# Optimization experiments

Hardware: AMD Instinct MI355X
Metric: run time of the kernel (lower is better)

Reference implementation:

```python
import jax, jax.numpy as jnp
import numpy as np

E = 200_000   # number of edges (messages)
T = 500_000   # number of triplets
H = 128       # hidden_channels
B = 8         # num_bilinear
R = 6         # num_radial
S = 7         # num_spherical


def setup_inputs() -> dict:
    key = jax.random.key(0)
    ks = jax.random.split(key, 18)
    w = 0.05  # small init scale for numerical stability
    return {
        "x":   jax.random.normal(ks[0], (E, H), dtype=jnp.float32),
        "rbf": jax.random.normal(ks[1], (E, R), dtype=jnp.float32),
        "sbf": jax.random.normal(ks[2], (T, S * R), dtype=jnp.float32),
        "idx_kj": jax.random.randint(ks[3], (T,), 0, E),
        "idx_ji": jax.random.randint(ks[4], (T,), 0, E),
        # parameters (stored as [in, out] so we apply x @ w)
        "lin_rbf_w": jax.random.normal(ks[5], (R, H), dtype=jnp.float32) * w,
        "lin_sbf_w": jax.random.normal(ks[6], (S * R, B), dtype=jnp.float32) * w,
        "lin_kj_w": jax.random.normal(ks[7], (H, H), dtype=jnp.float32) * w,
        "lin_kj_b": jnp.zeros((H,), dtype=jnp.float32),
        "lin_ji_w": jax.random.normal(ks[8], (H, H), dtype=jnp.float32) * w,
        "lin_ji_b": jnp.zeros((H,), dtype=jnp.float32),
        "W": jax.random.normal(ks[9], (H, B, H), dtype=jnp.float32) * (2.0 / H),
        "before_w": jax.random.normal(ks[10], (1, 2, H, H), dtype=jnp.float32) * w,
        "before_b": jnp.zeros((1, 2, H), dtype=jnp.float32),
        "lin_w": jax.random.normal(ks[11], (H, H), dtype=jnp.float32) * w,
        "lin_b": jnp.zeros((H,), dtype=jnp.float32),
        "after_w": jax.random.normal(ks[12], (2, 2, H, H), dtype=jnp.float32) * w,
        "after_b": jnp.zeros((2, 2, H), dtype=jnp.float32),
    }


def _residual(h, w2, b2):
    # DimeNet ResidualLayer: h + act(lin2(act(lin1(h))))
    return h + jax.nn.silu(jax.nn.silu(h @ w2[0] + b2[0]) @ w2[1] + b2[1])


def reference(x, rbf, sbf, idx_kj, idx_ji,
              lin_rbf_w, lin_sbf_w, lin_kj_w, lin_kj_b,
              lin_ji_w, lin_ji_b, W,
              before_w, before_b, lin_w, lin_b, after_w, after_b):
    act = jax.nn.silu
    rbf_p = rbf @ lin_rbf_w                     # [E, H]
    sbf_p = sbf @ lin_sbf_w                     # [T, B]
    x_ji = act(x @ lin_ji_w + lin_ji_b)         # [E, H]
    x_kj = act(x @ lin_kj_w + lin_kj_b) * rbf_p # [E, H]
    g = x_kj[idx_kj]                            # gather -> [T, H]
    # bilinear: 'wj,wl,ijl->wi' with i,l=hidden, j=bilinear
    m = jnp.einsum('wj,wl,ijl->wi', sbf_p, g, W)  # [T, H]
    agg = jax.ops.segment_sum(m, idx_ji, num_segments=x.shape[0])  # [E, H]
    h = x_ji + agg
    for i in range(before_w.shape[0]):
        h = _residual(h, before_w[i], before_b[i])
    h = act(h @ lin_w + lin_b) + x
    for i in range(after_w.shape[0]):
        h = _residual(h, after_w[i], after_b[i])
    return h
```

## Files before the change

kernel.cpp:

```cpp
#include <hip/hip_runtime.h>

#define E_N 200000
#define T_N 500000

typedef __attribute__((ext_vector_type(8))) short bf16x8;
typedef __attribute__((ext_vector_type(4))) float f32x4;
typedef unsigned short u16;
typedef unsigned int u32;

#define SWZ(b) ((b) ^ ((((b) >> 8) & 7) << 4))

__device__ __forceinline__ u16 f2bf(float f){
  u32 u = __float_as_uint(f);
  return (u16)((u + 0x7fffu + ((u >> 16) & 1u)) >> 16);
}
__device__ __forceinline__ float silu_f(float v){
  return __fdividef(v, 1.f + __expf(-v));
}
__device__ __forceinline__ void gl_lds16(const void* g, void* l){
  __builtin_amdgcn_global_load_lds((const __attribute__((address_space(1))) u32*)g,
                                   (__attribute__((address_space(3))) u32*)l, 16, 0, 0);
}

__device__ __forceinline__ void gemm_tile(const char* ldsA, const char* ldsB,
                                          int wv, int lane, f32x4 acc[8]){
  const int arow = wv*16 + (lane & 15);
  const int kof = (lane >> 4) << 3;
  #pragma unroll
  for (int kc = 0; kc < 4; kc++){
    const int kb = (kc*32 + kof)*2;
    bf16x8 a = *(const bf16x8*)(ldsA + SWZ(arow*256 + kb));
    #pragma unroll
    for (int n = 0; n < 8; n++){
      bf16x8 b = *(const bf16x8*)(ldsB + SWZ((n*16 + (lane & 15))*256 + kb));
      acc[n] = __builtin_amdgcn_mfma_f32_16x16x32_bf16(a, b, acc[n], 0, 0, 0);
    }
  }
}

__global__ __launch_bounds__(256) void k_cvt_W(const float* __restrict__ W, u16* __restrict__ out){
  int i = blockIdx.x*256 + threadIdx.x;
  out[i] = f2bf(W[i]);
}

__global__ __launch_bounds__(256) void k_cvt_T(const float* __restrict__ jiw, const float* __restrict__ kjw,
                                               const float* __restrict__ bw, const float* __restrict__ lw,
                                               const float* __restrict__ aw, u16* __restrict__ out){
  int i = blockIdx.x*256 + threadIdx.x;
  int m = i >> 14, o = i & 16383;
  int n = o >> 7, k = o & 127;
  const float* src;
  switch (m){
    case 0: src = jiw; break;
    case 1: src = kjw; break;
    case 2: src = bw; break;
    case 3: src = bw + 16384; break;
    case 4: src = lw; break;
    default: src = aw + (m - 5)*16384; break;
  }
  out[i] = f2bf(src[k*128 + n]);
}

__global__ __launch_bounds__(256) void k_edge(const float* __restrict__ x, const float* __restrict__ rbf,
    const float* __restrict__ rbfw, const u16* __restrict__ wji, const u16* __restrict__ wkj,
    const float* __restrict__ bji, const float* __restrict__ bkj,
    float* __restrict__ out, u16* __restrict__ xkj)
{
  __shared__ __align__(16) char ldsA[16384];
  __shared__ __align__(16) char ldsB[32768];
  __shared__ float lrbf[64*6];
  __shared__ float lrbfw[6*128];
  __shared__ float lbj[128];
  __shared__ float lbk[128];
  const int tid = threadIdx.x;
  const int e0 = blockIdx.x * 64;

  #pragma unroll
  for (int it = 0; it < 4; it++){
    int i = it*256 + tid;
    int row = i >> 4, c8 = (i & 15) << 3;
    const float4* s = (const float4*)(x + (e0 + row)*128 + c8);
    float4 v0 = s[0], v1 = s[1];
    union { u16 us[8]; uint4 q; } u;
    u.us[0]=f2bf(v0.x); u.us[1]=f2bf(v0.y); u.us[2]=f2bf(v0.z); u.us[3]=f2bf(v0.w);
    u.us[4]=f2bf(v1.x); u.us[5]=f2bf(v1.y); u.us[6]=f2bf(v1.z); u.us[7]=f2bf(v1.w);
    *(uint4*)(ldsA + SWZ(row*256 + c8*2)) = u.q;
  }
  #pragma unroll
  for (int it = 0; it < 8; it++){
    int p = (it*256 + tid)*16;
    int pb = __builtin_amdgcn_readfirstlane(p);
    int n = p >> 8, o = p & 255;
    gl_lds16((const char*)wji + n*256 + (o ^ ((n & 7) << 4)), ldsB + pb);
  }
  for (int i = tid; i < 384; i += 256) lrbf[i] = rbf[e0*6 + i];
  for (int i = tid; i < 768; i += 256) lrbfw[i] = rbfw[i];
  if (tid < 128){ lbj[tid] = bji[tid]; lbk[tid] = bkj[tid]; }
  __syncthreads();

  const int wv = tid >> 6, lane = tid & 63;
  const int colb = lane & 15, rgrp = (lane >> 4) << 2;
  f32x4 acc[8];
  #pragma unroll
  for (int n = 0; n < 8; n++)
    #pragma unroll
    for (int r = 0; r < 4; r++) acc[n][r] = 0.f;
  gemm_tile(ldsA, ldsB, wv, lane, acc);
  #pragma unroll
  for (int n = 0; n < 8; n++){
    int col = n*16 + colb;
    float b = lbj[col];
    #pragma unroll
    for (int r = 0; r < 4; r++){
      int row = e0 + wv*16 + rgrp + r;
      out[row*128 + col] = silu_f(acc[n][r] + b);
    }
  }
  __syncthreads();
  #pragma unroll
  for (int it = 0; it < 8; it++){
    int p = (it*256 + tid)*16;
    int pb = __builtin_amdgcn_readfirstlane(p);
    int n = p >> 8, o = p & 255;
    gl_lds16((const char*)wkj + n*256 + (o ^ ((n & 7) << 4)), ldsB + pb);
  }
  __syncthreads();
  #pragma unroll
  for (int n = 0; n < 8; n++)
    #pragma unroll
    for (int r = 0; r < 4; r++) acc[n][r] = 0.f;
  gemm_tile(ldsA, ldsB, wv, lane, acc);

  float rb[4][6];
  #pragma unroll
  for (int r = 0; r < 4; r++)
    #pragma unroll
    for (int c = 0; c < 6; c++) rb[r][c] = lrbf[(wv*16 + rgrp + r)*6 + c];
  #pragma unroll
  for (int n = 0; n < 8; n++){
    int col = n*16 + colb;
    float b = lbk[col];
    float wc[6];
    #pragma unroll
    for (int c = 0; c < 6; c++) wc[c] = lrbfw[c*128 + col];
    #pragma unroll
    for (int r = 0; r < 4; r++){
      float rp = 0.f;
      #pragma unroll
      for (int c = 0; c < 6; c++) rp += rb[r][c]*wc[c];
      int row = e0 + wv*16 + rgrp + r;
      xkj[row*128 + col] = f2bf(silu_f(acc[n][r] + b) * rp);
    }
  }
}

__global__ __launch_bounds__(512) void k_trip(
    const u16* __restrict__ xkj, const float* __restrict__ sbf, const float* __restrict__ sbfw,
    const int* __restrict__ idx_kj, const int* __restrict__ idx_ji, const u16* __restrict__ Wbf,
    float* __restrict__ out)
{
  __shared__ __align__(16) char ldsG[32768];
  __shared__ __align__(16) char ldsB[32768];
  __shared__ float lss[128*8];
  __shared__ int lji[128];
  __shared__ int lkj[128];
  const int tid = threadIdx.x;
  const int t0 = blockIdx.x * 128;

  {
    float* lsbf = (float*)ldsB;
    for (int i = tid; i < 128*42; i += 512){
      int gi = t0*42 + i;
      lsbf[i] = (gi < T_N*42) ? sbf[gi] : 0.f;
    }
  }
  if (tid < 128){
    int w = t0 + tid;
    lji[tid] = (w < T_N) ? idx_ji[w] : -1;
    lkj[tid] = (w < T_N) ? idx_kj[w] : 0;
  }
  __syncthreads();
  #pragma unroll
  for (int it = 0; it < 4; it++){
    int p = (it*512 + tid)*16;
    int pb = __builtin_amdgcn_readfirstlane(p);
    int w = p >> 8, o = p & 255;
    gl_lds16((const char*)xkj + lkj[w]*256 + (o ^ ((w & 7) << 4)), ldsG + pb);
  }
  {
    const float* lsbf = (const float*)ldsB;
    if (tid < 128){
      float a[8];
      #pragma unroll
      for (int k = 0; k < 8; k++) a[k] = 0.f;
      for (int c = 0; c < 42; c++){
        float v = lsbf[tid*42 + c];
        #pragma unroll
        for (int k = 0; k < 8; k++) a[k] += v * sbfw[c*8 + k];
      }
      #pragma unroll
      for (int k = 0; k < 8; k++) lss[tid*8 + k] = a[k];
    }
  }
  __syncthreads();
  #pragma unroll
  for (int it = 0; it < 4; it++){
    int p = (it*512 + tid)*16;
    int pb = __builtin_amdgcn_readfirstlane(p);
    int n = p >> 8, o = p & 255;
    gl_lds16((const char*)Wbf + n*2048 + (o ^ ((n & 7) << 4)), ldsB + pb);
  }
  __syncthreads();

  const int wv = tid >> 6, lane = tid & 63;
  const int rowl = wv*16 + (lane & 15);
  const int kof = (lane >> 4) << 3;
  f32x4 acc[8];
  #pragma unroll
  for (int n = 0; n < 8; n++)
    #pragma unroll
    for (int r = 0; r < 4; r++) acc[n][r] = 0.f;

  for (int j = 0; j < 8; j++){
    const float s = lss[rowl*8 + j];
    #pragma unroll
    for (int kc = 0; kc < 4; kc++){
      const int kb = (kc*32 + kof)*2;
      union { bf16x8 v; u32 u[4]; } ga, aa;
      ga.v = *(const bf16x8*)(ldsG + SWZ(rowl*256 + kb));
      #pragma unroll
      for (int q = 0; q < 4; q++){
        float lo = __uint_as_float(ga.u[q] << 16) * s;
        float hi = __uint_as_float(ga.u[q] & 0xffff0000u) * s;
        asm("v_cvt_pk_bf16_f32 %0, %1, %2" : "=v"(aa.u[q]) : "v"(lo), "v"(hi));
      }
      #pragma unroll
      for (int n = 0; n < 8; n++){
        bf16x8 b = *(const bf16x8*)(ldsB + SWZ((n*16 + (lane & 15))*256 + kb));
        acc[n] = __builtin_amdgcn_mfma_f32_16x16x32_bf16(aa.v, b, acc[n], 0, 0, 0);
      }
    }
    if (j < 7){
      __syncthreads();
      #pragma unroll
      for (int it = 0; it < 4; it++){
        int p = (it*512 + tid)*16;
        int pb = __builtin_amdgcn_readfirstlane(p);
        int n = p >> 8, o = p & 255;
        gl_lds16((const char*)Wbf + n*2048 + (j + 1)*256 + (o ^ ((n & 7) << 4)), ldsB + pb);
      }
      __syncthreads();
    }
  }
  const int colb = lane & 15, rgrp = (lane >> 4) << 2;
  #pragma unroll
  for (int n = 0; n < 8; n++){
    const int col = n*16 + colb;
    #pragma unroll
    for (int r = 0; r < 4; r++){
      int e = lji[wv*16 + rgrp + r];
      if (e >= 0) unsafeAtomicAdd(out + e*128 + col, acc[n][r]);
    }
  }
}

__global__ __launch_bounds__(256) void k_epi(
    const float* __restrict__ x, float* __restrict__ hio, const u16* __restrict__ wm,
    const float* __restrict__ bb2, const float* __restrict__ linb, const float* __restrict__ ab2)
{
  __shared__ __align__(16) char ldsA[16384];
  __shared__ __align__(16) char ldsB[32768];
  __shared__ float lbias[7][128];
  const int tid = threadIdx.x;
  const int e0 = blockIdx.x * 64;
  if (tid < 128){
    lbias[0][tid] = bb2[tid];
    lbias[1][tid] = bb2[128 + tid];
    lbias[2][tid] = linb[tid];
    lbias[3][tid] = ab2[tid];
    lbias[4][tid] = ab2[128 + tid];
    lbias[5][tid] = ab2[256 + tid];
    lbias[6][tid] = ab2[384 + tid];
  }
  const int wv = tid >> 6, lane = tid & 63;
  const int colb = lane & 15, rgrp = (lane >> 4) << 2;
  float h[8][4], t[8][4];
  f32x4 acc[8];
  #pragma unroll
  for (int n = 0; n < 8; n++)
    #pragma unroll
    for (int r = 0; r < 4; r++)
      h[n][r] = hio[(e0 + wv*16 + rgrp + r)*128 + n*16 + colb];

#define STAGE_B(mi) { \
  _Pragma("unroll") \
  for (int it = 0; it < 8; it++){ \
    int p = (it*256 + tid)*16; \
    int pb = __builtin_amdgcn_readfirstlane(p); \
    int nn = p >> 8, o = p & 255; \
    gl_lds16((const char*)wm + (mi)*32768 + nn*256 + (o ^ ((nn & 7) << 4)), ldsB + pb); \
  } }
#define WRITE_A(v) { \
  _Pragma("unroll") \
  for (int n = 0; n < 8; n++){ \
    _Pragma("unroll") \
    for (int r = 0; r < 4; r++){ \
      int rowl = wv*16 + rgrp + r; \
      *(u16*)(ldsA + SWZ(rowl*256 + (n*16 + colb)*2)) = f2bf(v[n][r]); \
    } } }
#define RUN_GEMM() { \
  _Pragma("unroll") \
  for (int n = 0; n < 8; n++){ \
    _Pragma("unroll") \
    for (int r = 0; r < 4; r++) acc[n][r] = 0.f; } \
  gemm_tile(ldsA, ldsB, wv, lane, acc); }

  STAGE_B(0); WRITE_A(h); __syncthreads(); RUN_GEMM();
  #pragma unroll
  for (int n = 0; n < 8; n++){ float b = lbias[0][n*16 + colb];
    #pragma unroll
    for (int r = 0; r < 4; r++) t[n][r] = silu_f(acc[n][r] + b); }
  __syncthreads(); STAGE_B(1); WRITE_A(t); __syncthreads(); RUN_GEMM();
  #pragma unroll
  for (int n = 0; n < 8; n++){ float b = lbias[1][n*16 + colb];
    #pragma unroll
    for (int r = 0; r < 4; r++) h[n][r] += silu_f(acc[n][r] + b); }
  __syncthreads(); STAGE_B(2); WRITE_A(h); __syncthreads(); RUN_GEMM();
  #pragma unroll
  for (int n = 0; n < 8; n++){ float b = lbias[2][n*16 + colb];
    #pragma unroll
    for (int r = 0; r < 4; r++)
      h[n][r] = silu_f(acc[n][r] + b) + x[(e0 + wv*16 + rgrp + r)*128 + n*16 + colb]; }
  __syncthreads(); STAGE_B(3); WRITE_A(h); __syncthreads(); RUN_GEMM();
  #pragma unroll
  for (int n = 0; n < 8; n++){ float b = lbias[3][n*16 + colb];
    #pragma unroll
    for (int r = 0; r < 4; r++) t[n][r] = silu_f(acc[n][r] + b); }
  __syncthreads(); STAGE_B(4); WRITE_A(t); __syncthreads(); RUN_GEMM();
  #pragma unroll
  for (int n = 0; n < 8; n++){ float b = lbias[4][n*16 + colb];
    #pragma unroll
    for (int r = 0; r < 4; r++) h[n][r] += silu_f(acc[n][r] + b); }
  __syncthreads(); STAGE_B(5); WRITE_A(h); __syncthreads(); RUN_GEMM();
  #pragma unroll
  for (int n = 0; n < 8; n++){ float b = lbias[5][n*16 + colb];
    #pragma unroll
    for (int r = 0; r < 4; r++) t[n][r] = silu_f(acc[n][r] + b); }
  __syncthreads(); STAGE_B(6); WRITE_A(t); __syncthreads(); RUN_GEMM();
  #pragma unroll
  for (int n = 0; n < 8; n++){ float b = lbias[6][n*16 + colb];
    #pragma unroll
    for (int r = 0; r < 4; r++) h[n][r] += silu_f(acc[n][r] + b); }

  #pragma unroll
  for (int n = 0; n < 8; n++)
    #pragma unroll
    for (int r = 0; r < 4; r++)
      hio[(e0 + wv*16 + rgrp + r)*128 + n*16 + colb] = h[n][r];
#undef STAGE_B
#undef WRITE_A
#undef RUN_GEMM
}

extern "C" void kernel_launch(void* const* d_in, const int* in_sizes, int n_in,
                              void* d_out, int out_size, void* d_ws, size_t ws_size,
                              hipStream_t stream)
{
  const float* x    = (const float*)d_in[0];
  const float* rbf  = (const float*)d_in[1];
  const float* sbf  = (const float*)d_in[2];
  const int* idx_kj = (const int*)d_in[3];
  const int* idx_ji = (const int*)d_in[4];
  const float* rbfw = (const float*)d_in[5];
  const float* sbfw = (const float*)d_in[6];
  const float* kjw  = (const float*)d_in[7];
  const float* kjb  = (const float*)d_in[8];
  const float* jiw  = (const float*)d_in[9];
  const float* jib  = (const float*)d_in[10];
  const float* W    = (const float*)d_in[11];
  const float* bw   = (const float*)d_in[12];
  const float* bb   = (const float*)d_in[13];
  const float* lw   = (const float*)d_in[14];
  const float* lb   = (const float*)d_in[15];
  const float* aw   = (const float*)d_in[16];
  const float* ab   = (const float*)d_in[17];
  float* out = (float*)d_out;
  char* ws = (char*)d_ws;
  u16* Wbf  = (u16*)(ws);
  u16* linT = (u16*)(ws + 262144);
  u16* xkj  = (u16*)(ws + 1048576);

  k_cvt_W<<<dim3(512), dim3(256), 0, stream>>>(W, Wbf);
  k_cvt_T<<<dim3(576), dim3(256), 0, stream>>>(jiw, kjw, bw, lw, aw, linT);
  k_edge<<<dim3(E_N/64), dim3(256), 0, stream>>>(x, rbf, rbfw, linT, linT + 16384, jib, kjb, out, xkj);
  k_trip<<<dim3((T_N + 127)/128), dim3(512), 0, stream>>>(xkj, sbf, sbfw, idx_kj, idx_ji, Wbf, out);
  k_epi<<<dim3(E_N/64), dim3(256), 0, stream>>>(x, out, linT + 2*16384, bb, lb, ab);
}
```

Before: 605.4 us.

## Double-buffer W slices, register-resident gathers, larger triplet tiles, prefetch epilogue weights

The triplet kernel now handles 256 triplets per block, with each wave owning two 16-row tiles. The gathered x_kj rows are held in registers instead of LDS, and W slices are double-buffered in LDS so the next slice loads while the current one is used for MFMA. This halves the barriers per slice, and each B fragment read from LDS now feeds two MFMAs. The epilogue kernel preloads the next layer's weights into registers during the current GEMM, then writes them to LDS, and both kernels gain occupancy hints in launch_bounds. The cost is higher register pressure, which could cause spills or lower occupancy.

```diff
diff --git a/kernel.cpp b/kernel.cpp
--- a/kernel.cpp
+++ b/kernel.cpp
@@ -20,6 +20,17 @@
 __device__ __forceinline__ void gl_lds16(const void* g, void* l){
   __builtin_amdgcn_global_load_lds((const __attribute__((address_space(1))) u32*)g,
                                    (__attribute__((address_space(3))) u32*)l, 16, 0, 0);
+}
+__device__ __forceinline__ bf16x8 scale8(uint4 g, float s){
+  union { bf16x8 v; u32 u[4]; } aa;
+  u32 gu[4] = { g.x, g.y, g.z, g.w };
+  #pragma unroll
+  for (int q = 0; q < 4; q++){
+    float lo = __uint_as_float(gu[q] << 16) * s;
+    float hi = __uint_as_float(gu[q] & 0xffff0000u) * s;
+    asm("v_cvt_pk_bf16_f32 %0, %1, %2" : "=v"(aa.u[q]) : "v"(lo), "v"(hi));
+  }
+  return aa.v;
 }
 
 __device__ __forceinline__ void gemm_tile(const char* ldsA, const char* ldsB,
@@ -154,117 +165,115 @@
   }
 }
 
-__global__ __launch_bounds__(512) void k_trip(
+__device__ __forceinline__ void stage_Wslice(const u16* __restrict__ Wbf, int j, char* dst, int tid){
+  #pragma unroll
+  for (int it = 0; it < 4; it++){
+    int p = (it*512 + tid)*16;
+    int pb = __builtin_amdgcn_readfirstlane(p);
+    int n = p >> 8, o = p & 255;
+    gl_lds16((const char*)Wbf + n*2048 + j*256 + (o ^ ((n & 7) << 4)), dst + pb);
+  }
+}
+
+__global__ __launch_bounds__(512, 4) void k_trip(
     const u16* __restrict__ xkj, const float* __restrict__ sbf, const float* __restrict__ sbfw,
     const int* __restrict__ idx_kj, const int* __restrict__ idx_ji, const u16* __restrict__ Wbf,
     float* __restrict__ out)
 {
-  __shared__ __align__(16) char ldsG[32768];
-  __shared__ __align__(16) char ldsB[32768];
-  __shared__ float lss[128*8];
-  __shared__ int lji[128];
-  __shared__ int lkj[128];
+  __shared__ __align__(16) char ldsW[2][32768];
+  __shared__ float lss[256*8];
+  __shared__ float lsw[336];
+  __shared__ int lji[256];
+  __shared__ int lkj[256];
   const int tid = threadIdx.x;
-  const int t0 = blockIdx.x * 128;
+  const int t0 = blockIdx.x * 256;
 
   {
-    float* lsbf = (float*)ldsB;
-    for (int i = tid; i < 128*42; i += 512){
+    float* scr = (float*)ldsW;
+    for (int i = tid; i < 256*42; i += 512){
       int gi = t0*42 + i;
-      lsbf[i] = (gi < T_N*42) ? sbf[gi] : 0.f;
-    }
-  }
-  if (tid < 128){
+      scr[i] = (gi < T_N*42) ? sbf[gi] : 0.f;
+    }
+  }
+  for (int i = tid; i < 336; i += 512) lsw[i] = sbfw[i];
+  if (tid < 256){
     int w = t0 + tid;
     lji[tid] = (w < T_N) ? idx_ji[w] : -1;
     lkj[tid] = (w < T_N) ? idx_kj[w] : 0;
   }
   __syncthreads();
-  #pragma unroll
-  for (int it = 0; it < 4; it++){
-    int p = (it*512 + tid)*16;
-    int pb = __builtin_amdgcn_readfirstlane(p);
-    int w = p >> 8, o = p & 255;
-    gl_lds16((const char*)xkj + lkj[w]*256 + (o ^ ((w & 7) << 4)), ldsG + pb);
-  }
-  {
-    const float* lsbf = (const float*)ldsB;
-    if (tid < 128){
-      float a[8];
+
+  const int wv = tid >> 6, lane = tid & 63;
+  const int r15 = lane & 15, q = lane >> 4;
+
+  uint4 graw[8];
+  #pragma unroll
+  for (int rt = 0; rt < 2; rt++){
+    int row = lkj[wv*32 + rt*16 + r15];
+    const char* src = (const char*)xkj + (long)row*256 + q*16;
+    #pragma unroll
+    for (int kc = 0; kc < 4; kc++)
+      graw[rt*4 + kc] = *(const uint4*)(src + kc*64);
+  }
+  if (tid < 256){
+    const float* scr = (const float*)ldsW;
+    float a[8];
+    #pragma unroll
+    for (int k = 0; k < 8; k++) a[k] = 0.f;
+    for (int c = 0; c < 42; c++){
+      float v = scr[tid*42 + c];
       #pragma unroll
-      for (int k = 0; k < 8; k++) a[k] = 0.f;
-      for (int c = 0; c < 42; c++){
-        float v = lsbf[tid*42 + c];
-        #pragma unroll
-        for (int k = 0; k < 8; k++) a[k] += v * sbfw[c*8 + k];
-      }
-      #pragma unroll
-      for (int k = 0; k < 8; k++) lss[tid*8 + k] = a[k];
-    }
-  }
-  __syncthreads();
-  #pragma unroll
-  for (int it = 0; it < 4; it++){
-    int p = (it*512 + tid)*16;
-    int pb = __builtin_amdgcn_readfirstlane(p);
-    int n = p >> 8, o = p & 255;
-    gl_lds16((const char*)Wbf + n*2048 + (o ^ ((n & 7) << 4)), ldsB + pb);
-  }
-  __syncthreads();
-
-  const int wv = tid >> 6, lane = tid & 63;
-  const int rowl = wv*16 + (lane & 15);
-  const int kof = (lane >> 4) << 3;
-  f32x4 acc[8];
+      for (int k = 0; k < 8; k++) a[k] += v * lsw[c*8 + k];
+    }
+    #pragma unroll
+    for (int k = 0; k < 8; k++) lss[tid*8 + k] = a[k];
+  }
+  __syncthreads();
+  stage_Wslice(Wbf, 0, ldsW[0], tid);
+  __syncthreads();
+
+  f32x4 acc0[8], acc1[8];
   #pragma unroll
   for (int n = 0; n < 8; n++)
     #pragma unroll
-    for (int r = 0; r < 4; r++) acc[n][r] = 0.f;
-
+    for (int r = 0; r < 4; r++){ acc0[n][r] = 0.f; acc1[n][r] = 0.f; }
+
+  const int swz_lane = (r15 & 7) << 4;
   for (int j = 0; j < 8; j++){
-    const float s = lss[rowl*8 + j];
+    const char* bp = ldsW[j & 1];
+    if (j < 7) stage_Wslice(Wbf, j + 1, ldsW[(j + 1) & 1], tid);
+    const float s0 = lss[(wv*32 + r15)*8 + j];
+    const float s1 = lss[(wv*32 + 16 + r15)*8 + j];
     #pragma unroll
     for (int kc = 0; kc < 4; kc++){
-      const int kb = (kc*32 + kof)*2;
-      union { bf16x8 v; u32 u[4]; } ga, aa;
-      ga.v = *(const bf16x8*)(ldsG + SWZ(rowl*256 + kb));
-      #pragma unroll
-      for (int q = 0; q < 4; q++){
-        float lo = __uint_as_float(ga.u[q] << 16) * s;
-        float hi = __uint_as_float(ga.u[q] & 0xffff0000u) * s;
-        asm("v_cvt_pk_bf16_f32 %0, %1, %2" : "=v"(aa.u[q]) : "v"(lo), "v"(hi));
-      }
+      const int ab = (r15*256 + q*16 + kc*64) ^ swz_lane;
+      bf16x8 aa0 = scale8(graw[kc], s0);
+      bf16x8 aa1 = scale8(graw[4 + kc], s1);
       #pragma unroll
       for (int n = 0; n < 8; n++){
-        bf16x8 b = *(const bf16x8*)(ldsB + SWZ((n*16 + (lane & 15))*256 + kb));
-        acc[n] = __builtin_amdgcn_mfma_f32_16x16x32_bf16(aa.v, b, acc[n], 0, 0, 0);
+        bf16x8 b = *(const bf16x8*)(bp + n*4096 + ab);
+        acc0[n] = __builtin_amdgcn_mfma_f32_16x16x32_bf16(aa0, b, acc0[n], 0, 0, 0);
+        acc1[n] = __builtin_amdgcn_mfma_f32_16x16x32_bf16(aa1, b, acc1[n], 0, 0, 0);
       }
     }
-    if (j < 7){
-      __syncthreads();
-      #pragma unroll
-      for (int it = 0; it < 4; it++){
-        int p = (it*512 + tid)*16;
-        int pb = __builtin_amdgcn_readfirstlane(p);
-        int n = p >> 8, o = p & 255;
-        gl_lds16((const char*)Wbf + n*2048 + (j + 1)*256 + (o ^ ((n & 7) << 4)), ldsB + pb);
-      }
-      __syncthreads();
-    }
-  }
-  const int colb = lane & 15, rgrp = (lane >> 4) << 2;
+    __syncthreads();
+  }
+
+  const int rgrp = q << 2;
   #pragma unroll
   for (int n = 0; n < 8; n++){
-    const int col = n*16 + colb;
+    const int col = n*16 + r15;
     #pragma unroll
     for (int r = 0; r < 4; r++){
-      int e = lji[wv*16 + rgrp + r];
-      if (e >= 0) unsafeAtomicAdd(out + e*128 + col, acc[n][r]);
-    }
-  }
-}
-
-__global__ __launch_bounds__(256) void k_epi(
+      int e0i = lji[wv*32 + rgrp + r];
+      if (e0i >= 0) unsafeAtomicAdd(out + e0i*128 + col, acc0[n][r]);
+      int e1i = lji[wv*32 + 16 + rgrp + r];
+      if (e1i >= 0) unsafeAtomicAdd(out + e1i*128 + col, acc1[n][r]);
+    }
+  }
+}
+
+__global__ __launch_bounds__(256, 3) void k_epi(
     const float* __restrict__ x, float* __restrict__ hio, const u16* __restrict__ wm,
     const float* __restrict__ bb2, const float* __restrict__ linb, const float* __restrict__ ab2)
 {
@@ -286,19 +295,33 @@
   const int colb = lane & 15, rgrp = (lane >> 4) << 2;
   float h[8][4], t[8][4];
   f32x4 acc[8];
+  uint4 rw[8];
   #pragma unroll
   for (int n = 0; n < 8; n++)
     #pragma unroll
     for (int r = 0; r < 4; r++)
       h[n][r] = hio[(e0 + wv*16 + rgrp + r)*128 + n*16 + colb];
 
-#define STAGE_B(mi) { \
+#define STAGE_B_GL(mi) { \
   _Pragma("unroll") \
   for (int it = 0; it < 8; it++){ \
     int p = (it*256 + tid)*16; \
     int pb = __builtin_amdgcn_readfirstlane(p); \
     int nn = p >> 8, o = p & 255; \
     gl_lds16((const char*)wm + (mi)*32768 + nn*256 + (o ^ ((nn & 7) << 4)), ldsB + pb); \
+  } }
+#define REG_LOAD_W(mi) { \
+  _Pragma("unroll") \
+  for (int it = 0; it < 8; it++){ \
+    int p = (it*256 + tid)*16; \
+    int nn = p >> 8, o = p & 255; \
+    rw[it] = *(const uint4*)((const char*)wm + (mi)*32768 + nn*256 + (o ^ ((nn & 7) << 4))); \
+  } }
+#define DS_WRITE_W() { \
+  _Pragma("unroll") \
+  for (int it = 0; it < 8; it++){ \
+    int p = (it*256 + tid)*16; \
+    *(uint4*)(ldsB + p) = rw[it]; \
   } }
 #define WRITE_A(v) { \
   _Pragma("unroll") \
@@ -314,52 +337,52 @@
     _Pragma("unroll") \
     for (int r = 0; r < 4; r++) acc[n][r] = 0.f; } \
   gemm_tile(ldsA, ldsB, wv, lane, acc); }
-
-  STAGE_B(0); WRITE_A(h); __syncthreads(); RUN_GEMM();
-  #pragma unroll
-  for (int n = 0; n < 8; n++){ float b = lbias[0][n*16 + colb];
-    #pragma unroll
-    for (int r = 0; r < 4; r++) t[n][r] = silu_f(acc[n][r] + b); }
-  __syncthreads(); STAGE_B(1); WRITE_A(t); __syncthreads(); RUN_GEMM();
-  #pragma unroll
-  for (int n = 0; n < 8; n++){ float b = lbias[1][n*16 + colb];
-    #pragma unroll
-    for (int r = 0; r < 4; r++) h[n][r] += silu_f(acc[n][r] + b); }
-  __syncthreads(); STAGE_B(2); WRITE_A(h); __syncthreads(); RUN_GEMM();
+#define EPI_T(bi) { \
+  _Pragma("unroll") \
+  for (int n = 0; n < 8; n++){ float b = lbias[bi][n*16 + colb]; \
+    _Pragma("unroll") \
+    for (int r = 0; r < 4; r++) t[n][r] = silu_f(acc[n][r] + b); } }
+#define EPI_H(bi) { \
+  _Pragma("unroll") \
+  for (int n = 0; n < 8; n++){ float b = lbias[bi][n*16 + colb]; \
+    _Pragma("unroll") \
+    for (int r = 0; r < 4; r++) h[n][r] += silu_f(acc[n][r] + b); } }
+
+  STAGE_B_GL(0);
+  REG_LOAD_W(1);
+  WRITE_A(h);
+  __syncthreads();
+  RUN_GEMM(); EPI_T(0);
+  __syncthreads(); DS_WRITE_W(); REG_LOAD_W(2); WRITE_A(t); __syncthreads();
+  RUN_GEMM(); EPI_H(1);
+  __syncthreads(); DS_WRITE_W(); REG_LOAD_W(3); WRITE_A(h); __syncthreads();
+  RUN_GEMM();
   #pragma unroll
   for (int n = 0; n < 8; n++){ float b = lbias[2][n*16 + colb];
     #pragma unroll
     for (int r = 0; r < 4; r++)
       h[n][r] = silu_f(acc[n][r] + b) + x[(e0 + wv*16 + rgrp + r)*128 + n*16 + colb]; }
-  __syncthreads(); STAGE_B(3); WRITE_A(h); __syncthreads(); RUN_GEMM();
-  #pragma unroll
-  for (int n = 0; n < 8; n++){ float b = lbias[3][n*16 + colb];
-    #pragma unroll
-    for (int r = 0; r < 4; r++) t[n][r] = silu_f(acc[n][r] + b); }
-  __syncthreads(); STAGE_B(4); WRITE_A(t); __syncthreads(); RUN_GEMM();
-  #pragma unroll
-  for (int n = 0; n < 8; n++){ float b = lbias[4][n*16 + colb];
-    #pragma unroll
-    for (int r = 0; r < 4; r++) h[n][r] += silu_f(acc[n][r] + b); }
-  __syncthreads(); STAGE_B(5); WRITE_A(h); __syncthreads(); RUN_GEMM();
-  #pragma unroll
-  for (int n = 0; n < 8; n++){ float b = lbias[5][n*16 + colb];
-    #pragma unroll
-    for (int r = 0; r < 4; r++) t[n][r] = silu_f(acc[n][r] + b); }
-  __syncthreads(); STAGE_B(6); WRITE_A(t); __syncthreads(); RUN_GEMM();
-  #pragma unroll
-  for (int n = 0; n < 8; n++){ float b = lbias[6][n*16 + colb];
-    #pragma unroll
-    for (int r = 0; r < 4; r++) h[n][r] += silu_f(acc[n][r] + b); }
+  __syncthreads(); DS_WRITE_W(); REG_LOAD_W(4); WRITE_A(h); __syncthreads();
+  RUN_GEMM(); EPI_T(3);
+  __syncthreads(); DS_WRITE_W(); REG_LOAD_W(5); WRITE_A(t); __syncthreads();
+  RUN_GEMM(); EPI_H(4);
+  __syncthreads(); DS_WRITE_W(); REG_LOAD_W(6); WRITE_A(h); __syncthreads();
+  RUN_GEMM(); EPI_T(5);
+  __syncthreads(); DS_WRITE_W(); WRITE_A(t); __syncthreads();
+  RUN_GEMM(); EPI_H(6);
 
   #pragma unroll
   for (int n = 0; n < 8; n++)
     #pragma unroll
     for (int r = 0; r < 4; r++)
       hio[(e0 + wv*16 + rgrp + r)*128 + n*16 + colb] = h[n][r];
-#undef STAGE_B
+#undef STAGE_B_GL
+#undef REG_LOAD_W
+#undef DS_WRITE_W
 #undef WRITE_A
 #undef RUN_GEMM
+#undef EPI_T
+#undef EPI_H
 }
 
 extern "C" void kernel_launch(void* const* d_in, const int* in_sizes, int n_in,
@@ -393,6 +416,6 @@
   k_cvt_W<<<dim3(512), dim3(256), 0, stream>>>(W, Wbf);
   k_cvt_T<<<dim3(576), dim3(256), 0, stream>>>(jiw, kjw, bw, lw, aw, linT);
   k_edge<<<dim3(E_N/64), dim3(256), 0, stream>>>(x, rbf, rbfw, linT, linT + 16384, jib, kjb, out, xkj);
-  k_trip<<<dim3((T_N + 127)/128), dim3(512), 0, stream>>>(xkj, sbf, sbfw, idx_kj, idx_ji, Wbf, out);
+  k_trip<<<dim3((T_N + 255)/256), dim3(512), 0, stream>>>(xkj, sbf, sbfw, idx_kj, idx_ji, Wbf, out);
   k_epi<<<dim3(E_N/64), dim3(256), 0, stream>>>(x, out, linT + 2*16384, bb, lb, ab);
 }
```

New measurement: 936.1 us. 54.6% more time.
